# Performance work log

Hardware: AMD Instinct MI355X
Metric: run time of the kernel (lower is better)

Reference implementation:

```python
import jax, jax.numpy as jnp
import numpy as np

B, C, H, W = 8, 256, 64, 64
EPS = 1e-5


def _mk_conv_bn(key, oc, ic):
    k = jax.random.split(key, 6)
    return dict(
        w=jax.random.normal(k[0], (oc, ic), jnp.float32) * 0.01,  # trunc-normal approx, stddev 0.01
        b=jnp.zeros((oc,), jnp.float32),
        s=jax.random.uniform(k[1], (oc,), jnp.float32, 0.5, 1.5),   # BN scale
        t=jax.random.normal(k[2], (oc,), jnp.float32) * 0.1,        # BN shift
        m=jax.random.normal(k[3], (oc,), jnp.float32) * 0.1,        # BN running mean
        v=jax.random.uniform(k[4], (oc,), jnp.float32, 0.5, 1.5),   # BN running var
    )


def setup_inputs() -> dict:
    key = jax.random.key(0)
    ks = jax.random.split(key, 6)
    d = {"x": jax.random.normal(ks[0], (B, C, H, W), jnp.float32)}
    for i, (oc, ic) in zip([1, 2, 3, 4], [(C // 8, C), (C // 8, C), (C // 2, C), (C, C // 2)]):
        p = _mk_conv_bn(ks[i], oc, ic)
        for name, val in p.items():
            d[f"{name}{i}"] = val
    d["gamma"] = jnp.asarray(0.5, jnp.float32)
    return d


def _cbn(x, w, b, s, t, m, v, relu=True):
    # conv1x1 + BatchNorm(eval) [+ ReLU]; dropout is identity at inference
    y = jnp.einsum('bchw,oc->bohw', x, w) + b[None, :, None, None]
    scale = (s / jnp.sqrt(v + EPS))[None, :, None, None]
    y = (y - m[None, :, None, None]) * scale + t[None, :, None, None]
    return jax.nn.relu(y) if relu else y


def _maxpool2(x):
    b, c, h, w = x.shape
    return x.reshape(b, c, h // 2, 2, w // 2, 2).max(axis=(3, 5))


def reference(x, w1, b1, s1, t1, m1, v1, w2, b2, s2, t2, m2, v2,
              w3, b3, s3, t3, m3, v3, w4, b4, s4, t4, m4, v4, gamma):
    b, c, h, w = x.shape
    f = _maxpool2(_cbn(x, w1, b1, s1, t1, m1, v1))   # (B, C/8, H/2, W/2)
    g = _cbn(x, w2, b2, s2, t2, m2, v2)              # (B, C/8, H, W)
    hh = _maxpool2(_cbn(x, w3, b3, s3, t3, m3, v3))  # (B, C/2, H/2, W/2)
    hw, hw4 = h * w, (h // 2) * (w // 2)
    f = f.reshape(b, c // 8, hw4).transpose(0, 2, 1)  # (B, HW/4, C/8)
    g = g.reshape(b, c // 8, hw)                      # (B, C/8, HW)
    s = jnp.einsum('bnk,bkm->bnm', f, g)              # (B, HW/4, HW)
    beta = jax.nn.softmax(s, axis=1)                  # softmax over dim=1, as in source
    hh = hh.reshape(b, c // 2, hw4)                   # (B, C/2, HW/4)
    o = jnp.einsum('bcn,bnm->bcm', hh, beta).reshape(b, c // 2, h, w)
    out = _cbn(o, w4, b4, s4, t4, m4, v4, relu=False)
    return gamma * out + x
```

## Files before the change

### kernel.cpp

```cpp
#include <hip/hip_runtime.h>
#include <hip/hip_bf16.h>

#define HW   4096
#define HW4  1024
#define EPS  1e-5f
#define SM_SHIFT 20.0f

typedef __attribute__((ext_vector_type(8))) short bf16x8;
typedef __attribute__((ext_vector_type(4))) float f32x4;

__device__ __forceinline__ short f2bs(float f) {
    union { float f; unsigned u; } v; v.f = f;
    unsigned r = v.u + 0x7FFFu + ((v.u >> 16) & 1u);
    return (short)(r >> 16);
}
__device__ __forceinline__ int swz64(int r, int c)  { return (r << 6) + ((c ^ (r & 7))  << 3); }
__device__ __forceinline__ int swz128(int r, int c) { return (r << 7) + ((c ^ (r & 15)) << 3); }
__device__ __forceinline__ int p40(int r, int c)    { return r * 40 + c * 8; }

__global__ __launch_bounds__(256) void conv123pool(
    const float* __restrict__ x,
    const float* __restrict__ w1, const float* __restrict__ b1, const float* __restrict__ s1,
    const float* __restrict__ t1, const float* __restrict__ m1, const float* __restrict__ v1,
    const float* __restrict__ w2, const float* __restrict__ b2, const float* __restrict__ s2,
    const float* __restrict__ t2, const float* __restrict__ m2, const float* __restrict__ v2,
    const float* __restrict__ w3, const float* __restrict__ b3, const float* __restrict__ s3,
    const float* __restrict__ t3, const float* __restrict__ m3, const float* __restrict__ v3,
    short* __restrict__ gbuf, short* __restrict__ fbuf, short* __restrict__ hhbuf)
{
    __shared__ __align__(16) short Wl[96 * 64];
    __shared__ __align__(16) short Xl[128 * 64];
    __shared__ float alB[96], beB[96];

    const int t = threadIdx.x;
    const int lane = t & 63, wv = t >> 6;
    const int quad = lane >> 4, l16 = lane & 15;
    const int ptile = blockIdx.x;
    const int ocg   = blockIdx.y;
    const int bz    = blockIdx.z;
    const int pBase = ptile * 128;
    const int wcol  = (wv & 1) * 32;
    const int woch  = (wv >> 1) * 48;

    if (t < 96) {
        int j = ocg * 96 + t;
        float pb, ps, ptv, pm, pv;
        if (j < 32)      { pb = b1[j]; ps = s1[j]; ptv = t1[j]; pm = m1[j]; pv = v1[j]; }
        else if (j < 64) { int c = j - 32; pb = b2[c]; ps = s2[c]; ptv = t2[c]; pm = m2[c]; pv = v2[c]; }
        else             { int c = j - 64; pb = b3[c]; ps = s3[c]; ptv = t3[c]; pm = m3[c]; pv = v3[c]; }
        float al = ps * rsqrtf(pv + EPS);
        alB[t] = al; beB[t] = (pb - pm) * al + ptv;
    }

    const f32x4 fzero = {0.f, 0.f, 0.f, 0.f};
    f32x4 acc[3][4];
    #pragma unroll
    for (int i = 0; i < 3; ++i)
        #pragma unroll
        for (int j = 0; j < 4; ++j) acc[i][j] = fzero;

    const int ptOff0 = wcol, ptOff1 = wcol + 16, ptOff2 = wcol + 64, ptOff3 = wcol + 80;
    const int xp  = t & 127, xk8 = t >> 7;

    for (int k0 = 0; k0 < 256; k0 += 64) {
        #pragma unroll
        for (int i = 0; i < 2; ++i) {
            int idx = t + i * 256;
            if (i == 0 || t < 128) {
                int oc = idx >> 2, kb = (idx & 3) * 16;
                int j = ocg * 96 + oc;
                const float* wp = (j < 32) ? (w1 + j * 256)
                                : (j < 64) ? (w2 + (j - 32) * 256)
                                           : (w3 + (j - 64) * 256);
                wp += k0 + kb;
                float4 a = *(const float4*)(wp);
                float4 b = *(const float4*)(wp + 4);
                float4 c = *(const float4*)(wp + 8);
                float4 d = *(const float4*)(wp + 12);
                bf16x8 lo, hi;
                lo[0]=f2bs(a.x); lo[1]=f2bs(a.y); lo[2]=f2bs(a.z); lo[3]=f2bs(a.w);
                lo[4]=f2bs(b.x); lo[5]=f2bs(b.y); lo[6]=f2bs(b.z); lo[7]=f2bs(b.w);
                hi[0]=f2bs(c.x); hi[1]=f2bs(c.y); hi[2]=f2bs(c.z); hi[3]=f2bs(c.w);
                hi[4]=f2bs(d.x); hi[5]=f2bs(d.y); hi[6]=f2bs(d.z); hi[7]=f2bs(d.w);
                *(bf16x8*)&Wl[swz64(oc, (kb >> 3))]     = lo;
                *(bf16x8*)&Wl[swz64(oc, (kb >> 3) + 1)] = hi;
            }
        }
        {
            const float* xp0 = x + ((size_t)bz * 256 + k0 + xk8 * 32) * HW + pBase + xp;
            float fv[32];
            #pragma unroll
            for (int i = 0; i < 32; ++i) fv[i] = xp0[(size_t)i * HW];
            #pragma unroll
            for (int c = 0; c < 4; ++c) {
                bf16x8 v;
                #pragma unroll
                for (int jj = 0; jj < 8; ++jj) v[jj] = f2bs(fv[c * 8 + jj]);
                *(bf16x8*)&Xl[swz64(xp, xk8 * 4 + c)] = v;
            }
        }
        __syncthreads();
        #pragma unroll
        for (int kk = 0; kk < 2; ++kk) {
            bf16x8 bfr[4];
            bfr[0] = *(const bf16x8*)&Xl[swz64(ptOff0 + l16, kk * 4 + quad)];
            bfr[1] = *(const bf16x8*)&Xl[swz64(ptOff1 + l16, kk * 4 + quad)];
            bfr[2] = *(const bf16x8*)&Xl[swz64(ptOff2 + l16, kk * 4 + quad)];
            bfr[3] = *(const bf16x8*)&Xl[swz64(ptOff3 + l16, kk * 4 + quad)];
            #pragma unroll
            for (int tt = 0; tt < 3; ++tt) {
                bf16x8 afr = *(const bf16x8*)&Wl[swz64(woch + tt * 16 + l16, kk * 4 + quad)];
                #pragma unroll
                for (int pt = 0; pt < 4; ++pt)
                    acc[tt][pt] = __builtin_amdgcn_mfma_f32_16x16x32_bf16(afr, bfr[pt], acc[tt][pt], 0, 0, 0);
            }
        }
        __syncthreads();
    }

    #pragma unroll
    for (int tt = 0; tt < 3; ++tt) {
        #pragma unroll
        for (int r = 0; r < 4; ++r) {
            int ocl = woch + tt * 16 + quad * 4 + r;
            int j = ocg * 96 + ocl;
            float al = alB[ocl], be = beB[ocl];
            float y[4];
            y[0] = fmaxf(acc[tt][0][r] * al + be, 0.f);
            y[1] = fmaxf(acc[tt][1][r] * al + be, 0.f);
            y[2] = fmaxf(acc[tt][2][r] * al + be, 0.f);
            y[3] = fmaxf(acc[tt][3][r] * al + be, 0.f);
            if (j >= 32 && j < 64) {
                size_t base = ((size_t)bz * 32 + (j - 32)) * HW + pBase;
                gbuf[base + ptOff0 + l16] = f2bs(y[0]);
                gbuf[base + ptOff1 + l16] = f2bs(y[1]);
                gbuf[base + ptOff2 + l16] = f2bs(y[2]);
                gbuf[base + ptOff3 + l16] = f2bs(y[3]);
            } else {
                #pragma unroll
                for (int c = 0; c < 2; ++c) {
                    float v  = fmaxf(y[c], y[c + 2]);
                    float po = fmaxf(v, __shfl_xor(v, 1));
                    if ((l16 & 1) == 0) {
                        int col = wcol + c * 16 + l16;
                        int n = ptile * 32 + (col >> 1);
                        if (j < 32) fbuf[((size_t)bz * 32 + j) * HW4 + n] = f2bs(po);
                        else        hhbuf[((size_t)bz * 128 + (j - 64)) * HW4 + n] = f2bs(po);
                    }
                }
            }
        }
    }
}

__global__ __launch_bounds__(256, 4) void attn_conv4(
    const short* __restrict__ gbuf,
    const short* __restrict__ fbuf,
    const short* __restrict__ hhbuf,
    const float* __restrict__ x,
    const float* __restrict__ w4, const float* __restrict__ b4, const float* __restrict__ s4,
    const float* __restrict__ t4, const float* __restrict__ m4, const float* __restrict__ v4,
    const float* __restrict__ gamma, float* __restrict__ out)
{
    __shared__ __align__(16) short smem[18432];
    __shared__ float alB4[256], beB4[256];
    short* gTl = smem;
    short* fTl = smem + 2560;
    short* sTl = smem + 5120;
    short* hhl = smem + 9216;
    short* o_l = smem;
    short* Wl4 = smem + 8192;

    const int t = threadIdx.x;
    const int lane = t & 63, wv = t >> 6;
    const int quad = lane >> 4, l16 = lane & 15;
    const int bz = blockIdx.y;
    const int m0 = blockIdx.x * 64;
    const int ms = wv * 16;
    const f32x4 fzero = {0.f, 0.f, 0.f, 0.f};

    {
        float al = s4[t] * rsqrtf(v4[t] + EPS);
        alB4[t] = al; beB4[t] = (b4[t] - m4[t]) * al + t4[t];
    }

    {
        int mm = t & 63, k8 = t >> 6;
        bf16x8 v;
        #pragma unroll
        for (int j = 0; j < 8; ++j)
            v[j] = gbuf[((size_t)bz * 32 + k8 * 8 + j) * HW + m0 + mm];
        *(bf16x8*)&gTl[p40(mm, k8)] = v;
    }
    __syncthreads();
    bf16x8 bg = *(const bf16x8*)&gTl[p40(ms + l16, quad)];

    const int fnn = t & 63, fk8 = t >> 6;
    const int hrow = t >> 3, hnc = t & 7;
    const short* fB = fbuf + (size_t)bz * 32 * HW4;
    const short* hB = hhbuf + (size_t)bz * 128 * HW4;

    float psum = 0.f;
    f32x4 oacc[8];
    #pragma unroll
    for (int i = 0; i < 8; ++i) oacc[i] = fzero;

    for (int n0 = 0; n0 < 1024; n0 += 64) {
        __syncthreads();
        {
            bf16x8 v;
            #pragma unroll
            for (int j = 0; j < 8; ++j)
                v[j] = fB[(fk8 * 8 + j) * HW4 + n0 + fnn];
            *(bf16x8*)&fTl[p40(fnn, fk8)] = v;
        }
        {
            #pragma unroll
            for (int i = 0; i < 4; ++i)
                *(bf16x8*)&hhl[swz64(i * 32 + hrow, hnc)] =
                    *(const bf16x8*)(hB + (size_t)(i * 32 + hrow) * HW4 + n0 + hnc * 8);
        }
        __syncthreads();

        f32x4 sacc[4];
        #pragma unroll
        for (int nt = 0; nt < 4; ++nt) {
            bf16x8 af = *(const bf16x8*)&fTl[p40(nt * 16 + l16, quad)];
            sacc[nt] = __builtin_amdgcn_mfma_f32_16x16x32_bf16(af, bg, fzero, 0, 0, 0);
        }

        #pragma unroll
        for (int nt = 0; nt < 4; ++nt) {
            short4 ev;
            #pragma unroll
            for (int r = 0; r < 4; ++r) {
                float e = __expf(sacc[nt][r] - SM_SHIFT);
                psum += e;
                ((short*)&ev)[r] = f2bs(e);
            }
            int chunk = nt * 2 + (quad >> 1);
            *(short4*)&sTl[swz64(ms + l16, chunk) + (quad & 1) * 4] = ev;
        }

        #pragma unroll
        for (int kk = 0; kk < 2; ++kk) {
            bf16x8 bs = *(const bf16x8*)&sTl[swz64(ms + l16, kk * 4 + quad)];
            #pragma unroll
            for (int ct = 0; ct < 8; ++ct) {
                bf16x8 ah = *(const bf16x8*)&hhl[swz64(ct * 16 + l16, kk * 4 + quad)];
                oacc[ct] = __builtin_amdgcn_mfma_f32_16x16x32_bf16(ah, bs, oacc[ct], 0, 0, 0);
            }
        }
    }
    __syncthreads();

    psum += __shfl_xor(psum, 16);
    psum += __shfl_xor(psum, 32);
    {
        float inv = 1.0f / psum;
        int m = ms + l16;
        #pragma unroll
        for (int ct = 0; ct < 8; ++ct) {
            short4 ov;
            #pragma unroll
            for (int r = 0; r < 4; ++r) ((short*)&ov)[r] = f2bs(oacc[ct][r] * inv);
            *(short4*)&o_l[swz128(m, ct * 2 + (quad >> 1)) + (quad & 1) * 4] = ov;
        }
    }

    f32x4 acc4[4][4];
    #pragma unroll
    for (int i = 0; i < 4; ++i)
        #pragma unroll
        for (int j = 0; j < 4; ++j) acc4[i][j] = fzero;

    #pragma unroll
    for (int k0 = 0; k0 < 128; k0 += 32) {
        __syncthreads();
        {
            const float* wp = w4 + t * 128 + k0;
            #pragma unroll
            for (int c = 0; c < 4; ++c) {
                float4 a = *(const float4*)(wp + c * 8);
                float4 b = *(const float4*)(wp + c * 8 + 4);
                bf16x8 v;
                v[0]=f2bs(a.x); v[1]=f2bs(a.y); v[2]=f2bs(a.z); v[3]=f2bs(a.w);
                v[4]=f2bs(b.x); v[5]=f2bs(b.y); v[6]=f2bs(b.z); v[7]=f2bs(b.w);
                *(bf16x8*)&Wl4[p40(t, c)] = v;
            }
        }
        __syncthreads();
        bf16x8 bfr[4];
        #pragma unroll
        for (int mt = 0; mt < 4; ++mt)
            bfr[mt] = *(const bf16x8*)&o_l[swz128(mt * 16 + l16, (k0 >> 3) + quad)];
        #pragma unroll
        for (int ot = 0; ot < 4; ++ot) {
            bf16x8 afr = *(const bf16x8*)&Wl4[p40(wv * 64 + ot * 16 + l16, quad)];
            #pragma unroll
            for (int mt = 0; mt < 4; ++mt)
                acc4[ot][mt] = __builtin_amdgcn_mfma_f32_16x16x32_bf16(afr, bfr[mt], acc4[ot][mt], 0, 0, 0);
        }
    }

    float gm = gamma[0];
    #pragma unroll
    for (int ot = 0; ot < 4; ++ot) {
        #pragma unroll
        for (int r = 0; r < 4; ++r) {
            int oc = wv * 64 + ot * 16 + quad * 4 + r;
            float al = alB4[oc], be = beB4[oc];
            #pragma unroll
            for (int mt = 0; mt < 4; ++mt) {
                int p = m0 + mt * 16 + l16;
                float y  = acc4[ot][mt][r] * al + be;
                float xo = x[((size_t)bz * 256 + oc) * HW + p];
                out[((size_t)bz * 256 + oc) * HW + p] = gm * y + xo;
            }
        }
    }
}

extern "C" void kernel_launch(void* const* d_in, const int* in_sizes, int n_in,
                              void* d_out, int out_size, void* d_ws, size_t ws_size,
                              hipStream_t stream)
{
    const float* x  = (const float*)d_in[0];
    const float* w1 = (const float*)d_in[1];
    const float* b1 = (const float*)d_in[2];
    const float* s1 = (const float*)d_in[3];
    const float* t1 = (const float*)d_in[4];
    const float* m1 = (const float*)d_in[5];
    const float* v1 = (const float*)d_in[6];
    const float* w2 = (const float*)d_in[7];
    const float* b2 = (const float*)d_in[8];
    const float* s2 = (const float*)d_in[9];
    const float* t2 = (const float*)d_in[10];
    const float* m2 = (const float*)d_in[11];
    const float* v2 = (const float*)d_in[12];
    const float* w3 = (const float*)d_in[13];
    const float* b3 = (const float*)d_in[14];
    const float* s3 = (const float*)d_in[15];
    const float* t3 = (const float*)d_in[16];
    const float* m3 = (const float*)d_in[17];
    const float* v3 = (const float*)d_in[18];
    const float* w4 = (const float*)d_in[19];
    const float* b4 = (const float*)d_in[20];
    const float* s4 = (const float*)d_in[21];
    const float* t4 = (const float*)d_in[22];
    const float* m4 = (const float*)d_in[23];
    const float* v4 = (const float*)d_in[24];
    const float* gm = (const float*)d_in[25];
    float* out = (float*)d_out;

    short* gbuf  = (short*)d_ws;
    short* fbuf  = gbuf  + (size_t)8 * 32 * 4096;
    short* hhbuf = fbuf  + (size_t)8 * 32 * 1024;

    conv123pool<<<dim3(32, 2, 8), 256, 0, stream>>>(
        x, w1, b1, s1, t1, m1, v1, w2, b2, s2, t2, m2, v2, w3, b3, s3, t3, m3, v3,
        gbuf, fbuf, hhbuf);
    attn_conv4<<<dim3(64, 8), 256, 0, stream>>>(
        gbuf, fbuf, hhbuf, x, w4, b4, s4, t4, m4, v4, gm, out);
}
```

Baseline: 172.3 us.

## Halve per-block tiles in both kernels to double grid size and occupancy

The conv kernel now gives each block 48 output channels instead of 96, launching four channel groups instead of two, and each wave covers a 16-column pixel slice. The attention kernel handles 32 query columns per block instead of 64 and splits the 128 hh channels across wave pairs, so the grid doubles to 1024 blocks and shared memory per block shrinks. The aim is more blocks and waves in flight to hide latency on the many CUs. The cost is that x is re-read and converted by twice as many conv blocks, the f/g/hh tiles and w4 are reloaded twice as often in attention, and each wave issues fewer MFMAs per LDS load.

```diff
diff --git a/kernel.cpp b/kernel.cpp
--- a/kernel.cpp
+++ b/kernel.cpp
@@ -18,7 +18,7 @@
 __device__ __forceinline__ int swz128(int r, int c) { return (r << 7) + ((c ^ (r & 15)) << 3); }
 __device__ __forceinline__ int p40(int r, int c)    { return r * 40 + c * 8; }
 
-__global__ __launch_bounds__(256) void conv123pool(
+__global__ __launch_bounds__(256, 4) void conv123pool(
     const float* __restrict__ x,
     const float* __restrict__ w1, const float* __restrict__ b1, const float* __restrict__ s1,
     const float* __restrict__ t1, const float* __restrict__ m1, const float* __restrict__ v1,
@@ -28,9 +28,9 @@
     const float* __restrict__ t3, const float* __restrict__ m3, const float* __restrict__ v3,
     short* __restrict__ gbuf, short* __restrict__ fbuf, short* __restrict__ hhbuf)
 {
-    __shared__ __align__(16) short Wl[96 * 64];
+    __shared__ __align__(16) short Wl[48 * 64];
     __shared__ __align__(16) short Xl[128 * 64];
-    __shared__ float alB[96], beB[96];
+    __shared__ float alB[48], beB[48];
 
     const int t = threadIdx.x;
     const int lane = t & 63, wv = t >> 6;
@@ -39,11 +39,9 @@
     const int ocg   = blockIdx.y;
     const int bz    = blockIdx.z;
     const int pBase = ptile * 128;
-    const int wcol  = (wv & 1) * 32;
-    const int woch  = (wv >> 1) * 48;
-
-    if (t < 96) {
-        int j = ocg * 96 + t;
+
+    if (t < 48) {
+        int j = ocg * 48 + t;
         float pb, ps, ptv, pm, pv;
         if (j < 32)      { pb = b1[j]; ps = s1[j]; ptv = t1[j]; pm = m1[j]; pv = v1[j]; }
         else if (j < 64) { int c = j - 32; pb = b2[c]; ps = s2[c]; ptv = t2[c]; pm = m2[c]; pv = v2[c]; }
@@ -53,100 +51,84 @@
     }
 
     const f32x4 fzero = {0.f, 0.f, 0.f, 0.f};
-    f32x4 acc[3][4];
-    #pragma unroll
-    for (int i = 0; i < 3; ++i)
-        #pragma unroll
-        for (int j = 0; j < 4; ++j) acc[i][j] = fzero;
-
-    const int ptOff0 = wcol, ptOff1 = wcol + 16, ptOff2 = wcol + 64, ptOff3 = wcol + 80;
+    f32x4 acc[3][2];
+    #pragma unroll
+    for (int i = 0; i < 3; ++i) { acc[i][0] = fzero; acc[i][1] = fzero; }
+
+    const int ptOff0 = wv * 16;
+    const int ptOff1 = 64 + wv * 16;
     const int xp  = t & 127, xk8 = t >> 7;
 
     for (int k0 = 0; k0 < 256; k0 += 64) {
-        #pragma unroll
-        for (int i = 0; i < 2; ++i) {
-            int idx = t + i * 256;
-            if (i == 0 || t < 128) {
-                int oc = idx >> 2, kb = (idx & 3) * 16;
-                int j = ocg * 96 + oc;
-                const float* wp = (j < 32) ? (w1 + j * 256)
-                                : (j < 64) ? (w2 + (j - 32) * 256)
-                                           : (w3 + (j - 64) * 256);
-                wp += k0 + kb;
-                float4 a = *(const float4*)(wp);
-                float4 b = *(const float4*)(wp + 4);
-                float4 c = *(const float4*)(wp + 8);
-                float4 d = *(const float4*)(wp + 12);
-                bf16x8 lo, hi;
-                lo[0]=f2bs(a.x); lo[1]=f2bs(a.y); lo[2]=f2bs(a.z); lo[3]=f2bs(a.w);
-                lo[4]=f2bs(b.x); lo[5]=f2bs(b.y); lo[6]=f2bs(b.z); lo[7]=f2bs(b.w);
-                hi[0]=f2bs(c.x); hi[1]=f2bs(c.y); hi[2]=f2bs(c.z); hi[3]=f2bs(c.w);
-                hi[4]=f2bs(d.x); hi[5]=f2bs(d.y); hi[6]=f2bs(d.z); hi[7]=f2bs(d.w);
-                *(bf16x8*)&Wl[swz64(oc, (kb >> 3))]     = lo;
-                *(bf16x8*)&Wl[swz64(oc, (kb >> 3) + 1)] = hi;
-            }
-        }
-        {
-            const float* xp0 = x + ((size_t)bz * 256 + k0 + xk8 * 32) * HW + pBase + xp;
-            float fv[32];
-            #pragma unroll
-            for (int i = 0; i < 32; ++i) fv[i] = xp0[(size_t)i * HW];
-            #pragma unroll
-            for (int c = 0; c < 4; ++c) {
+        if (t < 192) {
+            int oc = t >> 2, kb = (t & 3) * 16;
+            int j = ocg * 48 + oc;
+            const float* wp = (j < 32) ? (w1 + j * 256)
+                            : (j < 64) ? (w2 + (j - 32) * 256)
+                                       : (w3 + (j - 64) * 256);
+            wp += k0 + kb;
+            float4 a = *(const float4*)(wp);
+            float4 b = *(const float4*)(wp + 4);
+            float4 c = *(const float4*)(wp + 8);
+            float4 d = *(const float4*)(wp + 12);
+            bf16x8 lo, hi;
+            lo[0]=f2bs(a.x); lo[1]=f2bs(a.y); lo[2]=f2bs(a.z); lo[3]=f2bs(a.w);
+            lo[4]=f2bs(b.x); lo[5]=f2bs(b.y); lo[6]=f2bs(b.z); lo[7]=f2bs(b.w);
+            hi[0]=f2bs(c.x); hi[1]=f2bs(c.y); hi[2]=f2bs(c.z); hi[3]=f2bs(c.w);
+            hi[4]=f2bs(d.x); hi[5]=f2bs(d.y); hi[6]=f2bs(d.z); hi[7]=f2bs(d.w);
+            *(bf16x8*)&Wl[swz64(oc, (kb >> 3))]     = lo;
+            *(bf16x8*)&Wl[swz64(oc, (kb >> 3) + 1)] = hi;
+        }
+        #pragma unroll
+        for (int h = 0; h < 2; ++h) {
+            const float* xp0 = x + ((size_t)bz * 256 + k0 + xk8 * 32 + h * 16) * HW + pBase + xp;
+            float fv[16];
+            #pragma unroll
+            for (int i = 0; i < 16; ++i) fv[i] = xp0[(size_t)i * HW];
+            #pragma unroll
+            for (int c = 0; c < 2; ++c) {
                 bf16x8 v;
                 #pragma unroll
                 for (int jj = 0; jj < 8; ++jj) v[jj] = f2bs(fv[c * 8 + jj]);
-                *(bf16x8*)&Xl[swz64(xp, xk8 * 4 + c)] = v;
+                *(bf16x8*)&Xl[swz64(xp, xk8 * 4 + h * 2 + c)] = v;
             }
         }
         __syncthreads();
         #pragma unroll
         for (int kk = 0; kk < 2; ++kk) {
-            bf16x8 bfr[4];
-            bfr[0] = *(const bf16x8*)&Xl[swz64(ptOff0 + l16, kk * 4 + quad)];
-            bfr[1] = *(const bf16x8*)&Xl[swz64(ptOff1 + l16, kk * 4 + quad)];
-            bfr[2] = *(const bf16x8*)&Xl[swz64(ptOff2 + l16, kk * 4 + quad)];
-            bfr[3] = *(const bf16x8*)&Xl[swz64(ptOff3 + l16, kk * 4 + quad)];
+            bf16x8 bfr0 = *(const bf16x8*)&Xl[swz64(ptOff0 + l16, kk * 4 + quad)];
+            bf16x8 bfr1 = *(const bf16x8*)&Xl[swz64(ptOff1 + l16, kk * 4 + quad)];
             #pragma unroll
             for (int tt = 0; tt < 3; ++tt) {
-                bf16x8 afr = *(const bf16x8*)&Wl[swz64(woch + tt * 16 + l16, kk * 4 + quad)];
-                #pragma unroll
-                for (int pt = 0; pt < 4; ++pt)
-                    acc[tt][pt] = __builtin_amdgcn_mfma_f32_16x16x32_bf16(afr, bfr[pt], acc[tt][pt], 0, 0, 0);
-            }
-        }
-        __syncthreads();
-    }
-
+                bf16x8 afr = *(const bf16x8*)&Wl[swz64(tt * 16 + l16, kk * 4 + quad)];
+                acc[tt][0] = __builtin_amdgcn_mfma_f32_16x16x32_bf16(afr, bfr0, acc[tt][0], 0, 0, 0);
+                acc[tt][1] = __builtin_amdgcn_mfma_f32_16x16x32_bf16(afr, bfr1, acc[tt][1], 0, 0, 0);
+            }
+        }
+        __syncthreads();
+    }
+
+    const int col = wv * 16 + l16;
     #pragma unroll
     for (int tt = 0; tt < 3; ++tt) {
         #pragma unroll
         for (int r = 0; r < 4; ++r) {
-            int ocl = woch + tt * 16 + quad * 4 + r;
-            int j = ocg * 96 + ocl;
+            int ocl = tt * 16 + quad * 4 + r;
+            int j = ocg * 48 + ocl;
             float al = alB[ocl], be = beB[ocl];
-            float y[4];
-            y[0] = fmaxf(acc[tt][0][r] * al + be, 0.f);
-            y[1] = fmaxf(acc[tt][1][r] * al + be, 0.f);
-            y[2] = fmaxf(acc[tt][2][r] * al + be, 0.f);
-            y[3] = fmaxf(acc[tt][3][r] * al + be, 0.f);
+            float y0 = fmaxf(acc[tt][0][r] * al + be, 0.f);
+            float y1 = fmaxf(acc[tt][1][r] * al + be, 0.f);
             if (j >= 32 && j < 64) {
                 size_t base = ((size_t)bz * 32 + (j - 32)) * HW + pBase;
-                gbuf[base + ptOff0 + l16] = f2bs(y[0]);
-                gbuf[base + ptOff1 + l16] = f2bs(y[1]);
-                gbuf[base + ptOff2 + l16] = f2bs(y[2]);
-                gbuf[base + ptOff3 + l16] = f2bs(y[3]);
+                gbuf[base + col]      = f2bs(y0);
+                gbuf[base + 64 + col] = f2bs(y1);
             } else {
-                #pragma unroll
-                for (int c = 0; c < 2; ++c) {
-                    float v  = fmaxf(y[c], y[c + 2]);
-                    float po = fmaxf(v, __shfl_xor(v, 1));
-                    if ((l16 & 1) == 0) {
-                        int col = wcol + c * 16 + l16;
-                        int n = ptile * 32 + (col >> 1);
-                        if (j < 32) fbuf[((size_t)bz * 32 + j) * HW4 + n] = f2bs(po);
-                        else        hhbuf[((size_t)bz * 128 + (j - 64)) * HW4 + n] = f2bs(po);
-                    }
+                float v  = fmaxf(y0, y1);
+                float po = fmaxf(v, __shfl_xor(v, 1));
+                if ((l16 & 1) == 0) {
+                    int n = ptile * 32 + (col >> 1);
+                    if (j < 32) fbuf[((size_t)bz * 32 + j) * HW4 + n] = f2bs(po);
+                    else        hhbuf[((size_t)bz * 128 + (j - 64)) * HW4 + n] = f2bs(po);
                 }
             }
         }
@@ -162,21 +144,22 @@
     const float* __restrict__ t4, const float* __restrict__ m4, const float* __restrict__ v4,
     const float* __restrict__ gamma, float* __restrict__ out)
 {
-    __shared__ __align__(16) short smem[18432];
+    __shared__ __align__(16) short smem[14336];
     __shared__ float alB4[256], beB4[256];
     short* gTl = smem;
-    short* fTl = smem + 2560;
-    short* sTl = smem + 5120;
-    short* hhl = smem + 9216;
+    short* fTl = smem + 1280;
+    short* sTl = smem + 3840;
+    short* hhl = smem + 5888;
     short* o_l = smem;
-    short* Wl4 = smem + 8192;
+    short* Wl4 = smem + 4096;
 
     const int t = threadIdx.x;
     const int lane = t & 63, wv = t >> 6;
     const int quad = lane >> 4, l16 = lane & 15;
     const int bz = blockIdx.y;
-    const int m0 = blockIdx.x * 64;
-    const int ms = wv * 16;
+    const int m0 = blockIdx.x * 32;
+    const int ms = (wv >> 1) * 16;
+    const int ch = (wv & 1) * 64;
     const f32x4 fzero = {0.f, 0.f, 0.f, 0.f};
 
     {
@@ -184,8 +167,8 @@
         alB4[t] = al; beB4[t] = (b4[t] - m4[t]) * al + t4[t];
     }
 
-    {
-        int mm = t & 63, k8 = t >> 6;
+    if (t < 128) {
+        int mm = t & 31, k8 = t >> 5;
         bf16x8 v;
         #pragma unroll
         for (int j = 0; j < 8; ++j)
@@ -201,9 +184,9 @@
     const short* hB = hhbuf + (size_t)bz * 128 * HW4;
 
     float psum = 0.f;
-    f32x4 oacc[8];
-    #pragma unroll
-    for (int i = 0; i < 8; ++i) oacc[i] = fzero;
+    f32x4 oacc[4];
+    #pragma unroll
+    for (int i = 0; i < 4; ++i) oacc[i] = fzero;
 
     for (int n0 = 0; n0 < 1024; n0 += 64) {
         __syncthreads();
@@ -246,8 +229,8 @@
         for (int kk = 0; kk < 2; ++kk) {
             bf16x8 bs = *(const bf16x8*)&sTl[swz64(ms + l16, kk * 4 + quad)];
             #pragma unroll
-            for (int ct = 0; ct < 8; ++ct) {
-                bf16x8 ah = *(const bf16x8*)&hhl[swz64(ct * 16 + l16, kk * 4 + quad)];
+            for (int ct = 0; ct < 4; ++ct) {
+                bf16x8 ah = *(const bf16x8*)&hhl[swz64(ch + ct * 16 + l16, kk * 4 + quad)];
                 oacc[ct] = __builtin_amdgcn_mfma_f32_16x16x32_bf16(ah, bs, oacc[ct], 0, 0, 0);
             }
         }
@@ -260,19 +243,18 @@
         float inv = 1.0f / psum;
         int m = ms + l16;
         #pragma unroll
-        for (int ct = 0; ct < 8; ++ct) {
+        for (int ct = 0; ct < 4; ++ct) {
             short4 ov;
             #pragma unroll
             for (int r = 0; r < 4; ++r) ((short*)&ov)[r] = f2bs(oacc[ct][r] * inv);
-            *(short4*)&o_l[swz128(m, ct * 2 + (quad >> 1)) + (quad & 1) * 4] = ov;
-        }
-    }
-
-    f32x4 acc4[4][4];
-    #pragma unroll
-    for (int i = 0; i < 4; ++i)
-        #pragma unroll
-        for (int j = 0; j < 4; ++j) acc4[i][j] = fzero;
+            int chunk = (ch >> 3) + ct * 2 + (quad >> 1);
+            *(short4*)&o_l[swz128(m, chunk) + (quad & 1) * 4] = ov;
+        }
+    }
+
+    f32x4 acc4[4][2];
+    #pragma unroll
+    for (int i = 0; i < 4; ++i) { acc4[i][0] = fzero; acc4[i][1] = fzero; }
 
     #pragma unroll
     for (int k0 = 0; k0 < 128; k0 += 32) {
@@ -290,16 +272,13 @@
             }
         }
         __syncthreads();
-        bf16x8 bfr[4];
-        #pragma unroll
-        for (int mt = 0; mt < 4; ++mt)
-            bfr[mt] = *(const bf16x8*)&o_l[swz128(mt * 16 + l16, (k0 >> 3) + quad)];
+        bf16x8 bfr0 = *(const bf16x8*)&o_l[swz128(l16,      (k0 >> 3) + quad)];
+        bf16x8 bfr1 = *(const bf16x8*)&o_l[swz128(16 + l16, (k0 >> 3) + quad)];
         #pragma unroll
         for (int ot = 0; ot < 4; ++ot) {
             bf16x8 afr = *(const bf16x8*)&Wl4[p40(wv * 64 + ot * 16 + l16, quad)];
-            #pragma unroll
-            for (int mt = 0; mt < 4; ++mt)
-                acc4[ot][mt] = __builtin_amdgcn_mfma_f32_16x16x32_bf16(afr, bfr[mt], acc4[ot][mt], 0, 0, 0);
+            acc4[ot][0] = __builtin_amdgcn_mfma_f32_16x16x32_bf16(afr, bfr0, acc4[ot][0], 0, 0, 0);
+            acc4[ot][1] = __builtin_amdgcn_mfma_f32_16x16x32_bf16(afr, bfr1, acc4[ot][1], 0, 0, 0);
         }
     }
 
@@ -311,7 +290,7 @@
             int oc = wv * 64 + ot * 16 + quad * 4 + r;
             float al = alB4[oc], be = beB4[oc];
             #pragma unroll
-            for (int mt = 0; mt < 4; ++mt) {
+            for (int mt = 0; mt < 2; ++mt) {
                 int p = m0 + mt * 16 + l16;
                 float y  = acc4[ot][mt][r] * al + be;
                 float xo = x[((size_t)bz * 256 + oc) * HW + p];
@@ -357,9 +336,9 @@
     short* fbuf  = gbuf  + (size_t)8 * 32 * 4096;
     short* hhbuf = fbuf  + (size_t)8 * 32 * 1024;
 
-    conv123pool<<<dim3(32, 2, 8), 256, 0, stream>>>(
+    conv123pool<<<dim3(32, 4, 8), 256, 0, stream>>>(
         x, w1, b1, s1, t1, m1, v1, w2, b2, s2, t2, m2, v2, w3, b3, s3, t3, m3, v3,
         gbuf, fbuf, hhbuf);
-    attn_conv4<<<dim3(64, 8), 256, 0, stream>>>(
+    attn_conv4<<<dim3(128, 8), 256, 0, stream>>>(
         gbuf, fbuf, hhbuf, x, w4, b4, s4, t4, m4, v4, gm, out);
 }
```

After: 183.0 us. 1.06x slower.
